# Kernel tuning notes

Measured on AMD Instinct MI355X. Metric: run time of the kernel, lower is better.

Reference implementation:

```python
import jax, jax.numpy as jnp
import numpy as np

# region/recall params from layer config
NUM_CLASSES = 20
NUM_ANCHORS = 5
ANCHORS = jnp.array([[1.3221, 1.73145], [3.19275, 4.00944], [5.05587, 8.09892],
                     [9.47112, 4.84053], [11.2364, 10.0071]], dtype=jnp.float32)
CONF_THRESH = 0.5
NMS_THRESH = 0.45
IOU_THRESH = 0.5
EPS = 1e-6


def setup_inputs() -> dict:
    key = jax.random.key(0)
    k1, k2 = jax.random.split(key)
    output = jax.random.normal(k1, (8, NUM_ANCHORS * (5 + NUM_CLASSES), 19, 19), dtype=jnp.float32)
    target = jax.random.uniform(k2, (8, 250), dtype=jnp.float32)  # [B, 50*5] rows: cls,cx,cy,w,h
    return {"output": output, "target": target}


def decode_region_boxes(output):
    """get_region_boxes: anchor decode. output [B, A*(5+C), H, W] -> boxes [B, A*H*W, 4] cxcywh (normalized), det_conf [B, A*H*W]."""
    B, _, H, W = output.shape
    o = output.reshape(B, NUM_ANCHORS, 5 + NUM_CLASSES, H, W)
    gx = jnp.arange(W, dtype=output.dtype)
    gy = jnp.arange(H, dtype=output.dtype)
    cx = (jax.nn.sigmoid(o[:, :, 0]) + gx[None, None, None, :]) / W
    cy = (jax.nn.sigmoid(o[:, :, 1]) + gy[None, None, :, None]) / H
    bw = jnp.exp(o[:, :, 2]) * (ANCHORS[:, 0] / W)[None, :, None, None]
    bh = jnp.exp(o[:, :, 3]) * (ANCHORS[:, 1] / H)[None, :, None, None]
    det_conf = jax.nn.sigmoid(o[:, :, 4])
    boxes = jnp.stack([cx, cy, bw, bh], axis=-1).reshape(B, -1, 4)
    return boxes, det_conf.reshape(B, -1)


def pairwise_iou(a, b):
    """bbox_iou(x1y1x2y2=False) for all pairs. a [..., Na, 4], b [..., Nb, 4] cxcywh -> [..., Na, Nb]."""
    ax1 = (a[..., 0] - a[..., 2] * 0.5)[..., :, None]
    ax2 = (a[..., 0] + a[..., 2] * 0.5)[..., :, None]
    ay1 = (a[..., 1] - a[..., 3] * 0.5)[..., :, None]
    ay2 = (a[..., 1] + a[..., 3] * 0.5)[..., :, None]
    bx1 = (b[..., 0] - b[..., 2] * 0.5)[..., None, :]
    bx2 = (b[..., 0] + b[..., 2] * 0.5)[..., None, :]
    by1 = (b[..., 1] - b[..., 3] * 0.5)[..., None, :]
    by2 = (b[..., 1] + b[..., 3] * 0.5)[..., None, :]
    uw = jnp.maximum(ax2, bx2) - jnp.minimum(ax1, bx1)
    uh = jnp.maximum(ay2, by2) - jnp.minimum(ay1, by1)
    aw = a[..., 2][..., :, None]; ah = a[..., 3][..., :, None]
    bw = b[..., 2][..., None, :]; bh = b[..., 3][..., None, :]
    cw = aw + bw - uw
    ch = ah + bh - uh
    carea = jnp.where((cw > 0) & (ch > 0), cw * ch, 0.0)
    uarea = aw * ah + bw * bh - carea
    return carea / uarea


def greedy_nms_keep(iou_mat, valid):
    """Sequential greedy NMS over conf-sorted boxes using precomputed IoU. iou_mat [N,N], valid [N] bool."""
    N = valid.shape[0]
    idx = jnp.arange(N)
    def body(i, keep):
        sup = keep[i] & (iou_mat[i] > NMS_THRESH) & (idx > i)
        return keep & (~sup)
    return jax.lax.fori_loop(0, N, body, valid)


def reference(output, target):
    B = output.shape[0]
    boxes, det = decode_region_boxes(output)              # [B,N,4], [B,N]
    # sort by det_conf descending (nms sort order)
    order = jnp.argsort(-det, axis=1)
    boxes = jnp.take_along_axis(boxes, order[..., None], axis=1)
    det = jnp.take_along_axis(det, order, axis=1)
    valid = det > CONF_THRESH                             # boxes that enter nms (conf filter in get_region_boxes)
    iou_mat = pairwise_iou(boxes, boxes)                  # [B,N,N]
    keep = jax.vmap(greedy_nms_keep)(iou_mat, valid)      # [B,N]
    proposals = jnp.sum(keep)
    # ground truth: [B,T,5] rows [cls,cx,cy,w,h]; num_gts = boxes until first cx==0
    truths = target.reshape(B, -1, 5)
    gt_valid = jnp.cumprod((truths[..., 1] != 0).astype(jnp.int32), axis=1).astype(bool)  # [B,T]
    total = jnp.sum(gt_valid)
    iou_gt = pairwise_iou(truths[..., 1:5], boxes)        # [B,T,N]
    best_iou = jnp.max(jnp.where(keep[:, None, :], iou_gt, 0.0), axis=-1)  # [B,T]
    correct = jnp.sum(gt_valid & (best_iou > IOU_THRESH))
    total_f = total.astype(jnp.float32)
    prop_f = proposals.astype(jnp.float32)
    corr_f = correct.astype(jnp.float32)
    precision = corr_f / (prop_f + EPS)
    recall = corr_f / (total_f + EPS)
    fscore = 2.0 * precision * recall / (precision + recall + EPS)
    return jnp.stack([total_f, prop_f, corr_f, precision, recall, fscore])
```

## Files before the change

### kernel.cpp

```cpp
#include <hip/hip_runtime.h>

namespace {
constexpr int NA    = 5;
constexpr int NCELL = 361;
constexpr int NBOX  = 1805;
constexpr int KPAD  = 2048;
constexpr int TMAX  = 50;
constexpr float CONF_T = 0.5f;
constexpr float NMS_T  = 0.45f;
constexpr float IOU_T  = 0.5f;
constexpr int NWMAX   = 32;
constexpr int TRI_T   = 15;
constexpr int TRI_SEG = TRI_T * (TRI_T + 1) / 2;
constexpr int ROWPAD  = 1856;
constexpr int SOA_STRIDE = ROWPAD;
constexpr int SOA_ARR    = 8 * SOA_STRIDE;
constexpr size_t WS_COUNT = 0;
constexpr size_t WS_M     = 64;
constexpr size_t WS_SOA   = 256;
constexpr size_t WS_SUP   = 360448;
constexpr size_t WS_UBOX  = WS_SUP;
constexpr size_t WS_KEY   = WS_SUP + (1u << 20);
}

__device__ __constant__ float d_anchw[NA] = {1.3221f, 3.19275f, 5.05587f, 9.47112f, 11.2364f};
__device__ __constant__ float d_anchh[NA] = {1.73145f, 4.00944f, 8.09892f, 4.84053f, 10.0071f};

__device__ inline unsigned long long rdlane64(unsigned long long v, int l) {
    unsigned lo = (unsigned)__builtin_amdgcn_readlane((int)(unsigned)(v & 0xffffffffull), l);
    unsigned hi = (unsigned)__builtin_amdgcn_readlane((int)(unsigned)(v >> 32), l);
    return ((unsigned long long)hi << 32) | lo;
}

__global__ __launch_bounds__(256, 1) void k_decode(
    const float* __restrict__ net, float* __restrict__ ubox,
    unsigned long long* __restrict__ keyg, int* __restrict__ Marr,
    int* __restrict__ counters)
{
    __shared__ int sM;
    const int b = blockIdx.x, tid = threadIdx.x, lane = tid & 63;
    const float* op = net + (size_t)b * (NA * 25 * NCELL);
    if (tid == 0) sM = 0;
    if (b == 0 && tid < 4) counters[tid] = 0;
    __syncthreads();

    int cnt = 0;
    for (int n = tid; n < NBOX; n += 256) {
        int a = n / NCELL;
        int r = n - a * NCELL;
        int y = r / 19;
        int x = r - y * 19;
        int base = a * 25 * NCELL + r;
        float t0 = op[base];
        float t1 = op[base + 1 * NCELL];
        float t2 = op[base + 2 * NCELL];
        float t3 = op[base + 3 * NCELL];
        float t4 = op[base + 4 * NCELL];
        float cx = (1.0f / (1.0f + expf(-t0)) + (float)x) / 19.0f;
        float cy = (1.0f / (1.0f + expf(-t1)) + (float)y) / 19.0f;
        float bw = expf(t2) * (d_anchw[a] / 19.0f);
        float bh = expf(t3) * (d_anchh[a] / 19.0f);
        float det = 1.0f / (1.0f + expf(-t4));
        keyg[b * KPAD + n] = ((unsigned long long)(~__float_as_uint(det)) << 32) | (unsigned)n;
        ubox[0 * SOA_ARR + b * SOA_STRIDE + n] = cx - 0.5f * bw;
        ubox[1 * SOA_ARR + b * SOA_STRIDE + n] = cy - 0.5f * bh;
        ubox[2 * SOA_ARR + b * SOA_STRIDE + n] = cx + 0.5f * bw;
        ubox[3 * SOA_ARR + b * SOA_STRIDE + n] = cy + 0.5f * bh;
        ubox[4 * SOA_ARR + b * SOA_STRIDE + n] = bw;
        ubox[5 * SOA_ARR + b * SOA_STRIDE + n] = bh;
        cnt += (det > CONF_T) ? 1 : 0;
    }
    for (int n = NBOX + tid; n < KPAD; n += 256) keyg[b * KPAD + n] = ~0ull;
    for (int d = 32; d > 0; d >>= 1) cnt += __shfl_down(cnt, d, 64);
    if (lane == 0) atomicAdd(&sM, cnt);
    __syncthreads();
    if (tid == 0) Marr[b] = sM;
}

__global__ __launch_bounds__(256, 1) void k_rank(
    const unsigned long long* __restrict__ keyg, const float* __restrict__ ubox,
    float* __restrict__ soa)
{
    __shared__ unsigned long long lk[KPAD];
    const int blk = blockIdx.x, tid = threadIdx.x;
    const int b = blk & 7, wv = tid >> 6, lane = tid & 63;
    for (int i = tid; i < KPAD; i += 256) lk[i] = keyg[b * KPAD + i];
    __syncthreads();

    const int base = (blk >> 3) * 16 + wv * 4;
    unsigned long long kp[4];
    int cnt[4] = {0, 0, 0, 0};
    #pragma unroll
    for (int x = 0; x < 4; ++x) {
        int p = base + x;
        kp[x] = (p < NBOX) ? lk[p] : 0ull;
    }
    for (int c = 0; c < KPAD / 64; ++c) {
        unsigned long long q = lk[(c << 6) + lane];
        #pragma unroll
        for (int x = 0; x < 4; ++x)
            cnt[x] += __popcll(__ballot(q < kp[x]));
    }
    #pragma unroll
    for (int x = 0; x < 4; ++x) {
        int p = base + x;
        if (p < NBOX && lane < 6) {
            float v = ubox[lane * SOA_ARR + b * SOA_STRIDE + p];
            soa[lane * SOA_ARR + b * SOA_STRIDE + cnt[x]] = v;
        }
    }
}

__global__ __launch_bounds__(256) void k_iou_colT(
    const float* __restrict__ soa, const int* __restrict__ Marr,
    unsigned long long* __restrict__ supC)
{
    const int blk  = blockIdx.x;
    const int b    = blk & 7;
    const int lane = threadIdx.x & 63;
    const int j    = (blk >> 3) * 4 + (threadIdx.x >> 6);
    const int M = Marr[b];
    if (j >= M) return;
    const float* X1 = soa + 0 * SOA_ARR + b * SOA_STRIDE;
    const float* Y1 = soa + 1 * SOA_ARR + b * SOA_STRIDE;
    const float* X2 = soa + 2 * SOA_ARR + b * SOA_STRIDE;
    const float* Y2 = soa + 3 * SOA_ARR + b * SOA_STRIDE;
    const float* Wd = soa + 4 * SOA_ARR + b * SOA_STRIDE;
    const float* Hd = soa + 5 * SOA_ARR + b * SOA_STRIDE;
    const float bx1 = X1[j], by1 = Y1[j], bx2 = X2[j], by2 = Y2[j];
    const float bw = Wd[j], bh = Hd[j], barea = bw * bh;
    const int jw = j >> 6;
    unsigned long long* outp = supC + (size_t)b * 32 * ROWPAD + j;
    for (int t = 0; t <= jw; ++t) {
        int i = (t << 6) + lane;
        float ax1 = X1[i], ay1 = Y1[i], ax2 = X2[i], ay2 = Y2[i];
        float aw = Wd[i], ah = Hd[i];
        bool pred = false;
        if (i < j) {
            float uw = fmaxf(ax2, bx2) - fminf(ax1, bx1);
            float uh = fmaxf(ay2, by2) - fminf(ay1, by1);
            float cw = aw + bw - uw;
            float ch = ah + bh - uh;
            if (cw > 0.0f && ch > 0.0f) {
                float ca = cw * ch;
                float ua = aw * ah + barea - ca;
                pred = ca > NMS_T * ua;
            }
        }
        unsigned long long m = __ballot(pred);
        if (lane == 0) outp[(size_t)t * ROWPAD] = m;
    }
}

__global__ __launch_bounds__(512, 1) void k_sweep3(
    const float* __restrict__ soa, const float* __restrict__ tgt,
    const int* __restrict__ Marr, const unsigned long long* __restrict__ supC,
    int* __restrict__ counters, float* __restrict__ out)
{
    __shared__ unsigned long long tri[TRI_SEG * 64];
    __shared__ unsigned long long keepw[NWMAX];
    __shared__ int sNV, sCorr, sProp;
    const int b = blockIdx.x, tid = threadIdx.x;
    const int wv = tid >> 6, lane = tid & 63;
    const int M = Marr[b];
    const int nwa = (M + 63) >> 6;
    const unsigned long long* sb = supC + (size_t)b * 32 * ROWPAD;

    if (tid < NWMAX) keepw[tid] = 0ull;
    if (tid == 0) { sCorr = 0; sProp = 0; }

    const int tcap = (nwa < TRI_T) ? nwa : TRI_T;
    const int ntri = tcap * (tcap + 1) / 2;
    for (int seg = wv; seg < ntri; seg += 8) {
        int w = 0;
        while ((w + 1) * (w + 2) / 2 <= seg) ++w;
        int t = seg - w * (w + 1) / 2;
        tri[seg * 64 + lane] = sb[(size_t)t * ROWPAD + (w << 6) + lane];
    }
    if (wv == 1) {
        float cxv = (lane < TMAX) ? tgt[b * 250 + lane * 5 + 1] : 0.0f;
        unsigned long long bm = __ballot(cxv != 0.0f);
        unsigned long long inv = (~bm) & ((1ull << TMAX) - 1);
        if (lane == 0) sNV = inv ? (__ffsll((long long)inv) - 1) : TMAX;
    }
    __syncthreads();

    if (wv == 0 && nwa > 0) {
        unsigned long long rmv = 0, kwv = 0;
        int pcTot = 0;
        for (int t = 0; t < nwa; ++t) {
            unsigned long long cur = rdlane64(rmv, t);
            unsigned long long diag = (t < TRI_T)
                ? tri[(t * (t + 1) / 2 + t) * 64 + lane]
                : sb[(size_t)t * ROWPAD + (t << 6) + lane];
            int rem = M - (t << 6);
            unsigned long long vm = (rem >= 64) ? ~0ull : ((1ull << rem) - 1ull);
            unsigned long long live = vm & ~cur;
            while (live) {
                int i = __ffsll((long long)live) - 1;
                unsigned long long w64 = __ballot(((diag >> i) & 1ull) != 0ull);
                cur |= w64;
                live &= ~w64;
                live &= ~(1ull << i);
            }
            unsigned long long kp = vm & ~cur;
            pcTot += __popcll(kp);
            kwv = (lane == t) ? kp : kwv;
            for (int w = t + 1; w < nwa; ++w) {
                unsigned long long cw = (w < TRI_T)
                    ? tri[(w * (w + 1) / 2 + t) * 64 + lane]
                    : sb[(size_t)t * ROWPAD + (w << 6) + lane];
                unsigned long long m = __ballot((cw & kp) != 0ull);
                rmv = (lane == w) ? (rmv | m) : rmv;
            }
        }
        if (lane < NWMAX) keepw[lane] = (lane < nwa) ? kwv : 0ull;
        if (lane == 0) sProp = pcTot;
    }
    __syncthreads();

    const float* X1 = soa + 0 * SOA_ARR + b * SOA_STRIDE;
    const float* Y1 = soa + 1 * SOA_ARR + b * SOA_STRIDE;
    const float* X2 = soa + 2 * SOA_ARR + b * SOA_STRIDE;
    const float* Y2 = soa + 3 * SOA_ARR + b * SOA_STRIDE;
    const float* Wd = soa + 4 * SOA_ARR + b * SOA_STRIDE;
    const float* Hd = soa + 5 * SOA_ARR + b * SOA_STRIDE;
    const int nv = sNV;
    for (int t = wv; t < nv; t += 8) {
        const float* g = tgt + b * 250 + t * 5;
        float gcx = g[1], gcy = g[2], gw = g[3], gh = g[4];
        float gx1 = gcx - 0.5f * gw, gx2 = gcx + 0.5f * gw;
        float gy1 = gcy - 0.5f * gh, gy2 = gcy + 0.5f * gh;
        float garea = gw * gh;
        float best = 0.0f;
        for (int j0 = 0; j0 < M; j0 += 64) {
            int j = j0 + lane;
            bool ok = (j < M) && ((keepw[j0 >> 6] >> lane) & 1ull);
            int js = (j < NBOX) ? j : (NBOX - 1);
            float bw = Wd[js], bh = Hd[js];
            float uw = fmaxf(gx2, X2[js]) - fminf(gx1, X1[js]);
            float uh = fmaxf(gy2, Y2[js]) - fminf(gy1, Y1[js]);
            float cww = gw + bw - uw, chh = gh + bh - uh;
            float ca = (cww > 0.0f && chh > 0.0f) ? cww * chh : 0.0f;
            float ua = garea + bw * bh - ca;
            float iou = ca / ua;
            best = fmaxf(best, ok ? iou : 0.0f);
        }
        for (int d = 32; d > 0; d >>= 1) best = fmaxf(best, __shfl_down(best, d, 64));
        if (lane == 0 && best > IOU_T) atomicAdd(&sCorr, 1);
    }
    __syncthreads();

    if (tid == 0) {
        atomicAdd(counters + 0, sProp);
        atomicAdd(counters + 1, sCorr);
        atomicAdd(counters + 2, sNV);
        __threadfence();
        int done = atomicAdd(counters + 3, 1);
        if (done == 7) {
            float prop  = (float)atomicAdd(counters + 0, 0);
            float corr  = (float)atomicAdd(counters + 1, 0);
            float total = (float)atomicAdd(counters + 2, 0);
            float prec = corr / (prop + 1e-6f);
            float rec  = corr / (total + 1e-6f);
            float fs   = 2.0f * prec * rec / (prec + rec + 1e-6f);
            out[0] = total;
            out[1] = prop;
            out[2] = corr;
            out[3] = prec;
            out[4] = rec;
            out[5] = fs;
        }
    }
}

extern "C" void kernel_launch(void* const* d_in, const int* in_sizes, int n_in,
                              void* d_out, int out_size, void* d_ws, size_t ws_size,
                              hipStream_t stream) {
    const float* net = (const float*)d_in[0];
    const float* tgt = (const float*)d_in[1];
    char* ws = (char*)d_ws;
    int* counters = (int*)(ws + WS_COUNT);
    int* Marr     = (int*)(ws + WS_M);
    float* soa    = (float*)(ws + WS_SOA);
    float* ubox   = (float*)(ws + WS_UBOX);
    unsigned long long* keyg = (unsigned long long*)(ws + WS_KEY);
    unsigned long long* supC = (unsigned long long*)(ws + WS_SUP);

    k_decode<<<8, 256, 0, stream>>>(net, ubox, keyg, Marr, counters);
    k_rank<<<113 * 8, 256, 0, stream>>>(keyg, ubox, soa);
    k_iou_colT<<<452 * 8, 256, 0, stream>>>(soa, Marr, supC);
    k_sweep3<<<8, 512, 0, stream>>>(soa, tgt, Marr, supC, counters, (float*)d_out);
}
```

Measured before the change: 148.3 us.

## Parallelize greedy NMS sweep across waves with transposed diagonal blocks and compaction

Adds a kernel that computes transposed diagonal suppression blocks, so the serial wave resolves each intra-block suppression with a readlane instead of a ballot. The cross-block suppression updates move from wave 0 onto the other seven waves, which trail one block behind and synchronise once per block step. Only the most urgent next-block update stays on wave 0. Kept boxes are then compacted into shared memory, so the ground-truth IoU loop scans only kept boxes. This adds a kernel launch and a block-wide barrier per 64-box word.

```diff
diff --git a/kernel.cpp b/kernel.cpp
--- a/kernel.cpp
+++ b/kernel.cpp
@@ -10,8 +10,8 @@
 constexpr float NMS_T  = 0.45f;
 constexpr float IOU_T  = 0.5f;
 constexpr int NWMAX   = 32;
-constexpr int TRI_T   = 15;
-constexpr int TRI_SEG = TRI_T * (TRI_T + 1) / 2;
+constexpr int TCAP    = 15;
+constexpr int NLOW    = TCAP * (TCAP - 1) / 2;
 constexpr int ROWPAD  = 1856;
 constexpr int SOA_STRIDE = ROWPAD;
 constexpr int SOA_ARR    = 8 * SOA_STRIDE;
@@ -152,79 +152,177 @@
     }
 }
 
-__global__ __launch_bounds__(512, 1) void k_sweep3(
-    const float* __restrict__ soa, const float* __restrict__ tgt,
-    const int* __restrict__ Marr, const unsigned long long* __restrict__ supC,
-    int* __restrict__ counters, float* __restrict__ out)
-{
-    __shared__ unsigned long long tri[TRI_SEG * 64];
-    __shared__ unsigned long long keepw[NWMAX];
-    __shared__ int sNV, sCorr, sProp;
-    const int b = blockIdx.x, tid = threadIdx.x;
-    const int wv = tid >> 6, lane = tid & 63;
+__global__ __launch_bounds__(256) void k_diagT(
+    const float* __restrict__ soa, const int* __restrict__ Marr,
+    unsigned long long* __restrict__ supC)
+{
+    const int blk = blockIdx.x;
+    const int b   = blk & 7;
+    const int t   = blk >> 3;
+    const int wv  = threadIdx.x >> 6, lane = threadIdx.x & 63;
     const int M = Marr[b];
-    const int nwa = (M + 63) >> 6;
-    const unsigned long long* sb = supC + (size_t)b * 32 * ROWPAD;
-
-    if (tid < NWMAX) keepw[tid] = 0ull;
-    if (tid == 0) { sCorr = 0; sProp = 0; }
-
-    const int tcap = (nwa < TRI_T) ? nwa : TRI_T;
-    const int ntri = tcap * (tcap + 1) / 2;
-    for (int seg = wv; seg < ntri; seg += 8) {
-        int w = 0;
-        while ((w + 1) * (w + 2) / 2 <= seg) ++w;
-        int t = seg - w * (w + 1) / 2;
-        tri[seg * 64 + lane] = sb[(size_t)t * ROWPAD + (w << 6) + lane];
-    }
-    if (wv == 1) {
-        float cxv = (lane < TMAX) ? tgt[b * 250 + lane * 5 + 1] : 0.0f;
-        unsigned long long bm = __ballot(cxv != 0.0f);
-        unsigned long long inv = (~bm) & ((1ull << TMAX) - 1);
-        if (lane == 0) sNV = inv ? (__ffsll((long long)inv) - 1) : TMAX;
-    }
-    __syncthreads();
-
-    if (wv == 0 && nwa > 0) {
-        unsigned long long rmv = 0, kwv = 0;
-        int pcTot = 0;
-        for (int t = 0; t < nwa; ++t) {
-            unsigned long long cur = rdlane64(rmv, t);
-            unsigned long long diag = (t < TRI_T)
-                ? tri[(t * (t + 1) / 2 + t) * 64 + lane]
-                : sb[(size_t)t * ROWPAD + (t << 6) + lane];
-            int rem = M - (t << 6);
-            unsigned long long vm = (rem >= 64) ? ~0ull : ((1ull << rem) - 1ull);
-            unsigned long long live = vm & ~cur;
-            while (live) {
-                int i = __ffsll((long long)live) - 1;
-                unsigned long long w64 = __ballot(((diag >> i) & 1ull) != 0ull);
-                cur |= w64;
-                live &= ~w64;
-                live &= ~(1ull << i);
-            }
-            unsigned long long kp = vm & ~cur;
-            pcTot += __popcll(kp);
-            kwv = (lane == t) ? kp : kwv;
-            for (int w = t + 1; w < nwa; ++w) {
-                unsigned long long cw = (w < TRI_T)
-                    ? tri[(w * (w + 1) / 2 + t) * 64 + lane]
-                    : sb[(size_t)t * ROWPAD + (w << 6) + lane];
-                unsigned long long m = __ballot((cw & kp) != 0ull);
-                rmv = (lane == w) ? (rmv | m) : rmv;
-            }
-        }
-        if (lane < NWMAX) keepw[lane] = (lane < nwa) ? kwv : 0ull;
-        if (lane == 0) sProp = pcTot;
-    }
-    __syncthreads();
-
+    if ((t << 6) >= M) return;
     const float* X1 = soa + 0 * SOA_ARR + b * SOA_STRIDE;
     const float* Y1 = soa + 1 * SOA_ARR + b * SOA_STRIDE;
     const float* X2 = soa + 2 * SOA_ARR + b * SOA_STRIDE;
     const float* Y2 = soa + 3 * SOA_ARR + b * SOA_STRIDE;
     const float* Wd = soa + 4 * SOA_ARR + b * SOA_STRIDE;
     const float* Hd = soa + 5 * SOA_ARR + b * SOA_STRIDE;
+    const int j = (t << 6) + lane;
+    const float cx1 = X1[j], cy1 = Y1[j], cx2 = X2[j], cy2 = Y2[j];
+    const float cw0 = Wd[j], ch0 = Hd[j];
+    unsigned long long* supD = supC + ((size_t)b * 32 + 31) * ROWPAD;
+    for (int k = 0; k < 16; ++k) {
+        int i = (t << 6) + (wv << 4) + k;
+        float rx1 = X1[i], ry1 = Y1[i], rx2 = X2[i], ry2 = Y2[i];
+        float rw = Wd[i], rh = Hd[i], rarea = rw * rh;
+        bool pred = false;
+        if (i < j && j < M) {
+            float uw = fmaxf(rx2, cx2) - fminf(rx1, cx1);
+            float uh = fmaxf(ry2, cy2) - fminf(ry1, cy1);
+            float cw = rw + cw0 - uw;
+            float ch = rh + ch0 - uh;
+            if (cw > 0.0f && ch > 0.0f) {
+                float ca = cw * ch;
+                float ua = rarea + cw0 * ch0 - ca;
+                pred = ca > NMS_T * ua;
+            }
+        }
+        unsigned long long m = __ballot(pred);
+        if (lane == 0) supD[i] = m;
+    }
+}
+
+__global__ __launch_bounds__(512, 1) void k_sweep5(
+    const float* __restrict__ soa, const float* __restrict__ tgt,
+    const int* __restrict__ Marr, const unsigned long long* __restrict__ supC,
+    int* __restrict__ counters, float* __restrict__ out)
+{
+    __shared__ unsigned long long tri[(NLOW + TCAP) * 64];
+    __shared__ unsigned long long rmw[NWMAX], keepw[NWMAX];
+    __shared__ int offs[NWMAX];
+    __shared__ int sNV, sCorr, sProp, sK;
+    const int b = blockIdx.x, tid = threadIdx.x;
+    const int wv = tid >> 6, lane = tid & 63;
+    const int M = Marr[b];
+    const int nwa = (M + 63) >> 6;
+    const unsigned long long* sb = supC + (size_t)b * 32 * ROWPAD;
+    const unsigned long long* supD = sb + (size_t)31 * ROWPAD;
+
+    if (tid < NWMAX) { rmw[tid] = 0ull; keepw[tid] = 0ull; offs[tid] = 0; }
+    if (tid == 0) { sCorr = 0; sProp = 0; sK = 0; sNV = 0; }
+
+    const int tcap = (nwa < TCAP) ? nwa : TCAP;
+    const int nlow = tcap * (tcap - 1) / 2;
+    for (int s = wv; s < nlow + tcap; s += 8) {
+        if (s < nlow) {
+            int w = 1;
+            while ((w * (w + 1)) / 2 <= s) ++w;
+            int r = s - w * (w - 1) / 2;
+            tri[s * 64 + lane] = sb[(size_t)r * ROWPAD + (w << 6) + lane];
+        } else {
+            int t = s - nlow;
+            tri[(NLOW + t) * 64 + lane] = supD[(t << 6) + lane];
+        }
+    }
+    if (wv == 1) {
+        float cxv = (lane < TMAX) ? tgt[b * 250 + lane * 5 + 1] : 0.0f;
+        unsigned long long bm = __ballot(cxv != 0.0f);
+        unsigned long long inv = (~bm) & ((1ull << TMAX) - 1);
+        if (lane == 0) sNV = inv ? (__ffsll((long long)inv) - 1) : TMAX;
+    }
+
+    int ow[5]; int now = 0;
+    if (wv >= 1) {
+        for (int w = 2 + (wv - 1); w < nwa && now < 5; w += 7) ow[now++] = w;
+    }
+    __syncthreads();
+
+    unsigned long long urgent = 0;
+    int pcTot = 0;
+    unsigned long long diagv = 0;
+    if (wv == 0 && nwa > 0)
+        diagv = (0 < tcap) ? tri[NLOW * 64 + lane] : supD[lane];
+
+    for (int t = 0; t < nwa; ++t) {
+        if (wv == 0) {
+            unsigned long long rm = rmw[t] | urgent;
+            int rem = M - (t << 6);
+            unsigned long long vm = (rem >= 64) ? ~0ull : ((1ull << rem) - 1ull);
+            unsigned long long live = vm & ~rm;
+            while (live) {
+                int i = __ffsll((long long)live) - 1;
+                unsigned long long w = rdlane64(diagv, i);
+                rm |= w;
+                live &= ~w;
+                live &= ~(1ull << i);
+            }
+            unsigned long long kp = vm & ~rm;
+            pcTot += __popcll(kp);
+            if (lane == 0) keepw[t] = kp;
+            if (t + 1 < nwa) {
+                unsigned long long q = (t + 1 < tcap)
+                    ? tri[((t + 1) * t / 2 + t) * 64 + lane]
+                    : sb[(size_t)t * ROWPAD + ((t + 1) << 6) + lane];
+                urgent = __ballot((q & kp) != 0ull);
+                diagv = (t + 1 < tcap) ? tri[(NLOW + t + 1) * 64 + lane]
+                                       : supD[((t + 1) << 6) + lane];
+            }
+        } else if (t >= 1) {
+            unsigned long long km = keepw[t - 1];
+            #pragma unroll
+            for (int x = 0; x < 5; ++x) {
+                if (x < now) {
+                    int w = ow[x];
+                    if (w >= t + 1) {
+                        unsigned long long q = (w < tcap)
+                            ? tri[(w * (w - 1) / 2 + (t - 1)) * 64 + lane]
+                            : sb[(size_t)(t - 1) * ROWPAD + (w << 6) + lane];
+                        unsigned long long hit = __ballot((q & km) != 0ull);
+                        if (lane == 0 && hit) rmw[w] |= hit;
+                    }
+                }
+            }
+        }
+        __syncthreads();
+    }
+
+    if (wv == 0) {
+        int pc = (lane < nwa) ? __popcll(keepw[lane]) : 0;
+        int inc = pc;
+        for (int d = 1; d < 32; d <<= 1) {
+            int v = __shfl_up(inc, d, 64);
+            if (lane >= d) inc += v;
+        }
+        if (lane < nwa) offs[lane] = inc - pc;
+        if (nwa > 0 && lane == nwa - 1) sK = inc;
+        if (lane == 0) sProp = pcTot;
+    }
+    __syncthreads();
+
+    float* cb = reinterpret_cast<float*>(tri);
+    const float* X1 = soa + 0 * SOA_ARR + b * SOA_STRIDE;
+    const float* Y1 = soa + 1 * SOA_ARR + b * SOA_STRIDE;
+    const float* X2 = soa + 2 * SOA_ARR + b * SOA_STRIDE;
+    const float* Y2 = soa + 3 * SOA_ARR + b * SOA_STRIDE;
+    const float* Wd = soa + 4 * SOA_ARR + b * SOA_STRIDE;
+    const float* Hd = soa + 5 * SOA_ARR + b * SOA_STRIDE;
+    for (int j = tid; j < M; j += 512) {
+        int w = j >> 6;
+        unsigned long long kw = keepw[w];
+        if ((kw >> (j & 63)) & 1ull) {
+            int pos = offs[w] + __popcll(kw & ((1ull << (j & 63)) - 1ull));
+            cb[0 * 2048 + pos] = X1[j];
+            cb[1 * 2048 + pos] = Y1[j];
+            cb[2 * 2048 + pos] = X2[j];
+            cb[3 * 2048 + pos] = Y2[j];
+            cb[4 * 2048 + pos] = Wd[j];
+            cb[5 * 2048 + pos] = Hd[j];
+        }
+    }
+    __syncthreads();
+
+    const int K = sK;
     const int nv = sNV;
     for (int t = wv; t < nv; t += 8) {
         const float* g = tgt + b * 250 + t * 5;
@@ -233,13 +331,13 @@
         float gy1 = gcy - 0.5f * gh, gy2 = gcy + 0.5f * gh;
         float garea = gw * gh;
         float best = 0.0f;
-        for (int j0 = 0; j0 < M; j0 += 64) {
+        for (int j0 = 0; j0 < K; j0 += 64) {
             int j = j0 + lane;
-            bool ok = (j < M) && ((keepw[j0 >> 6] >> lane) & 1ull);
-            int js = (j < NBOX) ? j : (NBOX - 1);
-            float bw = Wd[js], bh = Hd[js];
-            float uw = fmaxf(gx2, X2[js]) - fminf(gx1, X1[js]);
-            float uh = fmaxf(gy2, Y2[js]) - fminf(gy1, Y1[js]);
+            bool ok = j < K;
+            int js = ok ? j : 0;
+            float bw = cb[4 * 2048 + js], bh = cb[5 * 2048 + js];
+            float uw = fmaxf(gx2, cb[2 * 2048 + js]) - fminf(gx1, cb[0 * 2048 + js]);
+            float uh = fmaxf(gy2, cb[3 * 2048 + js]) - fminf(gy1, cb[1 * 2048 + js]);
             float cww = gw + bw - uw, chh = gh + bh - uh;
             float ca = (cww > 0.0f && chh > 0.0f) ? cww * chh : 0.0f;
             float ua = garea + bw * bh - ca;
@@ -290,5 +388,6 @@
     k_decode<<<8, 256, 0, stream>>>(net, ubox, keyg, Marr, counters);
     k_rank<<<113 * 8, 256, 0, stream>>>(keyg, ubox, soa);
     k_iou_colT<<<452 * 8, 256, 0, stream>>>(soa, Marr, supC);
-    k_sweep3<<<8, 512, 0, stream>>>(soa, tgt, Marr, supC, counters, (float*)d_out);
-}
+    k_diagT<<<29 * 8, 256, 0, stream>>>(soa, Marr, supC);
+    k_sweep5<<<8, 512, 0, stream>>>(soa, tgt, Marr, supC, counters, (float*)d_out);
+}
```

Measured after the change: 148.7 us. No clear change (+0.3%).
